# Optimization experiments

Hardware: AMD Instinct MI355X
Metric: run time of the kernel (lower is better)

## Reference

```python
import jax, jax.numpy as jnp
from jax import lax
import numpy as np

N, T, D, H, HG, OG = 2048, 256, 16, 256, 256, 128

def setup_inputs() -> dict:
    key = jax.random.key(0)
    ks = jax.random.split(key, 16)
    s = 0.05
    return {
        'x':    jax.random.normal(ks[0], (N, T, D), jnp.float32),
        'Wih0': jax.random.normal(ks[1], (4 * H, D), jnp.float32) * s,
        'Whh0': jax.random.normal(ks[2], (4 * H, H), jnp.float32) * s,
        'bih0': jax.random.normal(ks[3], (4 * H,), jnp.float32) * s,
        'bhh0': jax.random.normal(ks[4], (4 * H,), jnp.float32) * s,
        'Wih1': jax.random.normal(ks[5], (4 * H, H), jnp.float32) * s,
        'Whh1': jax.random.normal(ks[6], (4 * H, H), jnp.float32) * s,
        'bih1': jax.random.normal(ks[7], (4 * H,), jnp.float32) * s,
        'bhh1': jax.random.normal(ks[8], (4 * H,), jnp.float32) * s,
        'Wg1':  jax.random.normal(ks[9], (H, HG), jnp.float32) * s,
        'Wg2':  jax.random.normal(ks[10], (HG, OG), jnp.float32) * s,
        'Wfc':  jax.random.normal(ks[11], (OG, 1), jnp.float32) * s,
        'bfc':  jax.random.normal(ks[12], (1,), jnp.float32) * s,
    }

def lstm_layer(x, Wih, Whh, bih, bhh):
    # x: [N, T, Din]; torch gate order i, f, g, o stacked along 4H
    n = x.shape[0]
    h4 = Whh.shape[0]
    hid = h4 // 4
    xg = jnp.einsum('ntd,gd->ntg', x, Wih) + bih + bhh  # precompute input part
    def step(carry, g_t):
        h, c = carry
        g = g_t + h @ Whh.T
        i, f, gg, o = jnp.split(g, 4, axis=-1)
        c = jax.nn.sigmoid(f) * c + jax.nn.sigmoid(i) * jnp.tanh(gg)
        h = jax.nn.sigmoid(o) * jnp.tanh(c)
        return (h, c), h
    h0 = jnp.zeros((n, hid), x.dtype)
    (_, _), hs = lax.scan(step, (h0, h0), jnp.swapaxes(xg, 0, 1))
    return jnp.swapaxes(hs, 0, 1)  # [N, T, H]

def adjacency(nf):
    # detached correlation graph + symmetric degree normalization
    f = lax.stop_gradient(nf)
    xc = f - f.mean(axis=1, keepdims=True)
    cov = xc @ xc.T
    d = jnp.sqrt(jnp.diag(cov))
    corr = jnp.nan_to_num(jnp.clip(cov / (d[:, None] * d[None, :]), -1.0, 1.0))
    A = corr + jnp.eye(f.shape[0], dtype=f.dtype)
    dinv = jnp.power(A.sum(axis=1), -0.5)
    dinv = jnp.where(jnp.isinf(dinv), 0.0, dinv)
    return dinv[:, None] * A * dinv[None, :]

def reference(x, Wih0, Whh0, bih0, bhh0, Wih1, Whh1, bih1, bhh1, Wg1, Wg2, Wfc, bfc):
    h = lstm_layer(x, Wih0, Whh0, bih0, bhh0)
    h = lstm_layer(h, Wih1, Whh1, bih1, bhh1)
    nf = h[:, -1, :]                      # [N, H]
    adj = adjacency(nf)                   # [N, N]
    g1 = jax.nn.relu(adj @ (nf @ Wg1))    # GCN layer 1 (dropout=0, eval)
    g2 = adj @ (g1 @ Wg2)                 # GCN layer 2
    pred = g2 @ Wfc + bfc                 # [N, 1]
    return pred[:, 0]
```

## Files before the change

kernel.cpp:

```cpp
#include <hip/hip_runtime.h>
#include <hip/hip_bf16.h>
#include <cmath>

#define NN 2048
#define TT 256
#define DD 16
#define HH 256
#define NBLK 512

typedef __attribute__((ext_vector_type(8))) short short8;
typedef __attribute__((ext_vector_type(4))) float f32x4;

__device__ __forceinline__ float sigmoidf_(float x){ return 1.0f/(1.0f+expf(-x)); }

__device__ __forceinline__ void glds16(const __hip_bfloat16* g, __hip_bfloat16* l){
  __builtin_amdgcn_global_load_lds(
      (const __attribute__((address_space(1))) void*)g,
      (__attribute__((address_space(3))) void*)l, 16, 0, 0);
}

__global__ __launch_bounds__(256) void pack_w2(const float* __restrict__ W,
                                               __hip_bfloat16* __restrict__ P){
  int tid = blockIdx.x*256 + threadIdx.x;
  int r = tid >> 8, k = tid & 255;
  float w = W[tid];
  __hip_bfloat16 h = __float2bfloat16(w);
  __hip_bfloat16 l = __float2bfloat16(w - __bfloat162float(h));
  size_t base = (size_t)r*512;
  P[base + k] = h; P[base + 256 + k] = l;
}
__global__ __launch_bounds__(256) void pack_w0(const float* __restrict__ W,
                                               __hip_bfloat16* __restrict__ P){
  int tid = blockIdx.x*256 + threadIdx.x;
  int r = tid >> 4, k = tid & 15;
  float w = W[tid];
  __hip_bfloat16 h = __float2bfloat16(w);
  __hip_bfloat16 l = __float2bfloat16(w - __bfloat162float(h));
  size_t base = (size_t)r*64;
  P[base + k] = h; P[base + 16 + k] = h; P[base + 32 + k] = l;
  P[base + 48 + k] = __float2bfloat16(0.0f);
}
__global__ __launch_bounds__(256) void pack_x(const float* __restrict__ x,
                                              __hip_bfloat16* __restrict__ Xp){
  int tid = blockIdx.x*256 + threadIdx.x;
  const float* xr = x + (size_t)tid*16;
  __hip_bfloat16* o = Xp + (size_t)tid*64;
  for (int k=0;k<16;k++){
    float v = xr[k];
    __hip_bfloat16 h = __float2bfloat16(v);
    __hip_bfloat16 l = __float2bfloat16(v - __bfloat162float(h));
    o[k] = h; o[16+k] = l; o[32+k] = h; o[48+k] = __float2bfloat16(0.0f);
  }
}
__global__ __launch_bounds__(256) void recon_nf(const __hip_bfloat16* __restrict__ hi,
    const __hip_bfloat16* __restrict__ lo, float* __restrict__ nf){
  int tid = blockIdx.x*256 + threadIdx.x;
  nf[tid] = __bfloat162float(hi[tid]) + __bfloat162float(lo[tid]);
}

__global__ __launch_bounds__(256) void bar_init(unsigned* __restrict__ bar){
  for (int i = threadIdx.x; i < 2048; i += 256) bar[i] = 0u;
}

__device__ __forceinline__ void lean_sync(unsigned* bar, int t, int bid){
  __syncthreads();
  if (threadIdx.x == 0){
    const int x = bid & 7;
    unsigned a = __hip_atomic_fetch_add(bar + x*16, 1u, __ATOMIC_RELAXED,
                                        __HIP_MEMORY_SCOPE_AGENT);
    if (a == (unsigned)(64u*(t+1) - 1u)){
      asm volatile("buffer_wbl2 sc1\n\ts_waitcnt vmcnt(0)" ::: "memory");
      unsigned g = __hip_atomic_fetch_add(bar + 128, 1u, __ATOMIC_RELAXED,
                                          __HIP_MEMORY_SCOPE_AGENT);
      if (g == (unsigned)(8u*(t+1) - 1u)){
        #pragma unroll
        for (int i=0;i<16;i++)
          __hip_atomic_store(bar + 256 + i*64, (unsigned)(t+1),
                             __ATOMIC_RELAXED, __HIP_MEMORY_SCOPE_AGENT);
      } else {
        while (__hip_atomic_load(bar + 256 + x*64, __ATOMIC_RELAXED,
                                 __HIP_MEMORY_SCOPE_AGENT) < (unsigned)(t+1))
          __builtin_amdgcn_s_sleep(8);
      }
      asm volatile("buffer_inv sc1\n\ts_waitcnt vmcnt(0)" ::: "memory");
      __hip_atomic_store(bar + 1536 + x*64, (unsigned)(t+1),
                         __ATOMIC_RELAXED, __HIP_MEMORY_SCOPE_AGENT);
    } else {
      while (__hip_atomic_load(bar + 1536 + x*64, __ATOMIC_RELAXED,
                               __HIP_MEMORY_SCOPE_AGENT) < (unsigned)(t+1))
        __builtin_amdgcn_s_sleep(4);
    }
  }
  __syncthreads();
  asm volatile("buffer_inv\n\ts_waitcnt vmcnt(0)" ::: "memory");
}

__device__ __forceinline__ void mm_merged(
    const __hip_bfloat16* __restrict__ Ahi, const __hip_bfloat16* __restrict__ Alo,
    size_t lda,
    const __hip_bfloat16* __restrict__ Bhi, const __hip_bfloat16* __restrict__ Blo,
    size_t ldb, int Klen,
    int m0, int j0, int wv, int lane, int rr, int sw8, int frow,
    f32x4 (&acc)[2][4],
    __hip_bfloat16* AsH, __hip_bfloat16* AsL,
    __hip_bfloat16* BsH, __hip_bfloat16* BsL)
{
  const size_t arow = (size_t)(m0 + wv*32 + rr)*lda + sw8;
  const size_t brow = (size_t)(wv*256 + j0 + rr)*ldb + sw8;
  for (int kb=0; kb<Klen; kb+=64){
    {
      const __hip_bfloat16* AbH = Ahi + arow + kb;
      __hip_bfloat16* AdH = AsH + (wv*32)*64;
      #pragma unroll
      for (int c2=0;c2<4;c2++) glds16(AbH + (size_t)(c2*8)*lda, AdH + c2*8*64);
      const __hip_bfloat16* AbL = Alo + arow + kb;
      __hip_bfloat16* AdL = AsL + (wv*32)*64;
      #pragma unroll
      for (int c2=0;c2<4;c2++) glds16(AbL + (size_t)(c2*8)*lda, AdL + c2*8*64);
      const __hip_bfloat16* Bb1 = Bhi + brow + kb;
      __hip_bfloat16* Bd1 = BsH + (wv<<4)*64;
      glds16(Bb1, Bd1); glds16(Bb1 + (size_t)8*ldb, Bd1 + 8*64);
      const __hip_bfloat16* Bb2 = Blo + brow + kb;
      __hip_bfloat16* Bd2 = BsL + (wv<<4)*64;
      glds16(Bb2, Bd2); glds16(Bb2 + (size_t)8*ldb, Bd2 + 8*64);
    }
    __syncthreads();
    #pragma unroll
    for (int w2=0; w2<2; ++w2){
      const int sl8 = ((((w2<<2) + (lane>>4)) ^ (lane&7)) << 3);
      short8 ah0 = *(const short8*)&AsH[(wv*32 +      frow)*64 + sl8];
      short8 ah1 = *(const short8*)&AsH[(wv*32 + 16 + frow)*64 + sl8];
      short8 al0 = *(const short8*)&AsL[(wv*32 +      frow)*64 + sl8];
      short8 al1 = *(const short8*)&AsL[(wv*32 + 16 + frow)*64 + sl8];
      #pragma unroll
      for (int g=0; g<4; ++g){
        short8 bh = *(const short8*)&BsH[((g<<4) + frow)*64 + sl8];
        acc[0][g] = __builtin_amdgcn_mfma_f32_16x16x32_bf16(ah0, bh, acc[0][g], 0,0,0);
        acc[1][g] = __builtin_amdgcn_mfma_f32_16x16x32_bf16(ah1, bh, acc[1][g], 0,0,0);
        acc[0][g] = __builtin_amdgcn_mfma_f32_16x16x32_bf16(al0, bh, acc[0][g], 0,0,0);
        acc[1][g] = __builtin_amdgcn_mfma_f32_16x16x32_bf16(al1, bh, acc[1][g], 0,0,0);
        short8 bl = *(const short8*)&BsL[((g<<4) + frow)*64 + sl8];
        acc[0][g] = __builtin_amdgcn_mfma_f32_16x16x32_bf16(ah0, bl, acc[0][g], 0,0,0);
        acc[1][g] = __builtin_amdgcn_mfma_f32_16x16x32_bf16(ah1, bl, acc[1][g], 0,0,0);
      }
    }
    __syncthreads();
  }
}

__device__ __forceinline__ void mm_single64(
    const __hip_bfloat16* __restrict__ A, size_t lda,
    const __hip_bfloat16* __restrict__ B, size_t ldb,
    int m0, int j0, int wv, int lane, int rr, int sw8, int frow,
    f32x4 (&acc)[2][4],
    __hip_bfloat16* As0, __hip_bfloat16* Bh0)
{
  {
    const __hip_bfloat16* Ab = A + (size_t)(m0 + wv*32 + rr)*lda + sw8;
    __hip_bfloat16* Ad = As0 + (wv*32)*64;
    #pragma unroll
    for (int c2=0;c2<4;c2++) glds16(Ab + (size_t)(c2*8)*lda, Ad + c2*8*64);
    const __hip_bfloat16* Bb1 = B + (size_t)(wv*256 + j0 + rr)*ldb + sw8;
    __hip_bfloat16* Bd1 = Bh0 + (wv<<4)*64;
    glds16(Bb1, Bd1); glds16(Bb1 + (size_t)8*ldb, Bd1 + 8*64);
  }
  __syncthreads();
  #pragma unroll
  for (int w2=0; w2<2; ++w2){
    const int sl8 = ((((w2<<2) + (lane>>4)) ^ (lane&7)) << 3);
    short8 a0 = *(const short8*)&As0[(wv*32 +      frow)*64 + sl8];
    short8 a1 = *(const short8*)&As0[(wv*32 + 16 + frow)*64 + sl8];
    #pragma unroll
    for (int g=0; g<4; ++g){
      short8 b1 = *(const short8*)&Bh0[((g<<4) + frow)*64 + sl8];
      acc[0][g] = __builtin_amdgcn_mfma_f32_16x16x32_bf16(a0, b1, acc[0][g], 0,0,0);
      acc[1][g] = __builtin_amdgcn_mfma_f32_16x16x32_bf16(a1, b1, acc[1][g], 0,0,0);
    }
  }
  __syncthreads();
}

__global__ __launch_bounds__(256, 2) void lstm2_all(
    const __hip_bfloat16* __restrict__ Xp,
    const __hip_bfloat16* __restrict__ P0ih,
    const __hip_bfloat16* __restrict__ P0hh,
    const __hip_bfloat16* __restrict__ P1ih,
    const __hip_bfloat16* __restrict__ P1hh,
    const float* __restrict__ bih0, const float* __restrict__ bhh0,
    const float* __restrict__ bih1, const float* __restrict__ bhh1,
    __hip_bfloat16* __restrict__ H0hi0, __hip_bfloat16* __restrict__ H0lo0,
    __hip_bfloat16* __restrict__ H0hi1, __hip_bfloat16* __restrict__ H0lo1,
    __hip_bfloat16* __restrict__ H1hi0, __hip_bfloat16* __restrict__ H1lo0,
    __hip_bfloat16* __restrict__ H1hi1, __hip_bfloat16* __restrict__ H1lo1,
    unsigned* __restrict__ bar)
{
  __shared__ __align__(16) __hip_bfloat16 AsH[128*64];
  __shared__ __align__(16) __hip_bfloat16 AsL[128*64];
  __shared__ __align__(16) __hip_bfloat16 BsH[64*64];
  __shared__ __align__(16) __hip_bfloat16 BsL[64*64];

  const int bid = blockIdx.x;
  const int xcd = bid & 7;
  const int slot = bid >> 3;
  const bool isL0 = xcd < 4;
  const int lg = isL0 ? xcd : (xcd - 4);
  const int jg = ((lg & 1) << 3) + (slot & 7);
  const int mg = ((lg >> 1) << 3) + (slot >> 3);
  const int m0 = mg << 7;
  const int j0 = jg << 4;
  const int lane = threadIdx.x & 63, wv = threadIdx.x >> 6;
  const int rr = lane >> 3;
  const int sw8 = (((lane & 7) ^ rr) << 3);
  const int frow = lane & 15;

  const int j = j0 + frow;
  const float* bih = isL0 ? bih0 : bih1;
  const float* bhh = isL0 ? bhh0 : bhh1;
  const float b0 = bih[j]        + bhh[j];
  const float b1 = bih[HH + j]   + bhh[HH + j];
  const float b2 = bih[2*HH + j] + bhh[2*HH + j];
  const float b3 = bih[3*HH + j] + bhh[3*HH + j];

  float creg[2][4] = {{0.f,0.f,0.f,0.f},{0.f,0.f,0.f,0.f}};

  for (int t = 0; t <= TT; ++t){
    const int p = t & 1;
    const bool active = isL0 ? (t < TT) : (t >= 1);
    if (active){
      f32x4 acc[2][4] = {};
      const __hip_bfloat16* h0p_hi = p ? H0hi0 : H0hi1;
      const __hip_bfloat16* h0p_lo = p ? H0lo0 : H0lo1;
      if (isL0){
        if (t != 0){
          mm_merged(h0p_hi, h0p_lo, 256, P0hh, P0hh+256, 512, 256,
                    m0, j0, wv, lane, rr, sw8, frow, acc, AsH, AsL, BsH, BsL);
        }
        mm_single64(Xp + (size_t)t*64, (size_t)TT*64, P0ih, 64,
                    m0, j0, wv, lane, rr, sw8, frow, acc, AsH, BsH);
      } else {
        mm_merged(h0p_hi, h0p_lo, 256, P1ih, P1ih+256, 512, 256,
                  m0, j0, wv, lane, rr, sw8, frow, acc, AsH, AsL, BsH, BsL);
        if (t != 1){
          const __hip_bfloat16* h1p_hi = p ? H1hi1 : H1hi0;
          const __hip_bfloat16* h1p_lo = p ? H1lo1 : H1lo0;
          mm_merged(h1p_hi, h1p_lo, 256, P1hh, P1hh+256, 512, 256,
                    m0, j0, wv, lane, rr, sw8, frow, acc, AsH, AsL, BsH, BsL);
        }
      }
      __hip_bfloat16* ohi = isL0 ? (p ? H0hi1 : H0hi0)
                                 : (p ? H1hi0 : H1hi1);
      __hip_bfloat16* olo = isL0 ? (p ? H0lo1 : H0lo0)
                                 : (p ? H1lo0 : H1lo1);
      #pragma unroll
      for (int mt=0; mt<2; ++mt){
        const int mrb = m0 + wv*32 + mt*16 + ((lane>>4)<<2);
        #pragma unroll
        for (int r=0; r<4; ++r){
          const size_t mi = (size_t)(mrb + r)*HH + j;
          float gi = acc[mt][0][r] + b0;
          float gf = acc[mt][1][r] + b1;
          float gg = acc[mt][2][r] + b2;
          float go = acc[mt][3][r] + b3;
          float cn = sigmoidf_(gf)*creg[mt][r] + sigmoidf_(gi)*tanhf(gg);
          creg[mt][r] = cn;
          float hv = sigmoidf_(go)*tanhf(cn);
          __hip_bfloat16 hb = __float2bfloat16(hv);
          ohi[mi] = hb;
          olo[mi] = __float2bfloat16(hv - __bfloat162float(hb));
        }
      }
    }
    if (t < TT) lean_sync(bar, t, bid);
  }
}

__global__ __launch_bounds__(256) void gemm_nn(
    float* __restrict__ C, const float* __restrict__ A, const float* __restrict__ B,
    int K, int lda, int ldb, int ldc, int relu)
{
  __shared__ float As_[16][68];
  __shared__ float Bs_[16][64];
  float acc[4][4] = {};
  const int tx = threadIdx.x;
  const int m0 = blockIdx.y<<6, n0 = blockIdx.x<<6;
  const int am = tx>>2, ak = (tx&3)<<2;
  const int bk = tx>>4, bn = (tx&15)<<2;
  const int mm = (tx>>4)<<2, nc = (tx&15)<<2;
  for (int kb=0; kb<K; kb+=16){
    float4 av = *reinterpret_cast<const float4*>(A + (size_t)(m0+am)*lda + kb + ak);
    As_[ak][am]=av.x; As_[ak+1][am]=av.y; As_[ak+2][am]=av.z; As_[ak+3][am]=av.w;
    *reinterpret_cast<float4*>(&Bs_[bk][bn]) =
      *reinterpret_cast<const float4*>(B + (size_t)(kb+bk)*ldb + n0 + bn);
    __syncthreads();
    #pragma unroll
    for (int k=0;k<16;k++){
      float4 a4 = *reinterpret_cast<const float4*>(&As_[k][mm]);
      float4 b4 = *reinterpret_cast<const float4*>(&Bs_[k][nc]);
      acc[0][0]=fmaf(a4.x,b4.x,acc[0][0]); acc[0][1]=fmaf(a4.x,b4.y,acc[0][1]);
      acc[0][2]=fmaf(a4.x,b4.z,acc[0][2]); acc[0][3]=fmaf(a4.x,b4.w,acc[0][3]);
      acc[1][0]=fmaf(a4.y,b4.x,acc[1][0]); acc[1][1]=fmaf(a4.y,b4.y,acc[1][1]);
      acc[1][2]=fmaf(a4.y,b4.z,acc[1][2]); acc[1][3]=fmaf(a4.y,b4.w,acc[1][3]);
      acc[2][0]=fmaf(a4.z,b4.x,acc[2][0]); acc[2][1]=fmaf(a4.z,b4.y,acc[2][1]);
      acc[2][2]=fmaf(a4.z,b4.z,acc[2][2]); acc[2][3]=fmaf(a4.z,b4.w,acc[2][3]);
      acc[3][0]=fmaf(a4.w,b4.x,acc[3][0]); acc[3][1]=fmaf(a4.w,b4.y,acc[3][1]);
      acc[3][2]=fmaf(a4.w,b4.z,acc[3][2]); acc[3][3]=fmaf(a4.w,b4.w,acc[3][3]);
    }
    __syncthreads();
  }
  #pragma unroll
  for (int r=0;r<4;r++){
    float4 v = make_float4(acc[r][0],acc[r][1],acc[r][2],acc[r][3]);
    if (relu){ v.x=fmaxf(v.x,0.f); v.y=fmaxf(v.y,0.f); v.z=fmaxf(v.z,0.f); v.w=fmaxf(v.w,0.f); }
    *reinterpret_cast<float4*>(C + (size_t)(m0+mm+r)*ldc + n0 + nc) = v;
  }
}

__global__ __launch_bounds__(256) void gemm_nt(
    float* __restrict__ C, const float* __restrict__ A, const float* __restrict__ B,
    int K, int lda, int ldb, int ldc)
{
  __shared__ float As_[16][68];
  __shared__ float Bs_[16][68];
  float acc[4][4] = {};
  const int tx = threadIdx.x;
  const int m0 = blockIdx.y<<6, n0 = blockIdx.x<<6;
  const int am = tx>>2, ak = (tx&3)<<2;
  const int mm = (tx>>4)<<2, nc = (tx&15)<<2;
  for (int kb=0; kb<K; kb+=16){
    float4 av = *reinterpret_cast<const float4*>(A + (size_t)(m0+am)*lda + kb + ak);
    As_[ak][am]=av.x; As_[ak+1][am]=av.y; As_[ak+2][am]=av.z; As_[ak+3][am]=av.w;
    float4 bv = *reinterpret_cast<const float4*>(B + (size_t)(n0+am)*ldb + kb + ak);
    Bs_[ak][am]=bv.x; Bs_[ak+1][am]=bv.y; Bs_[ak+2][am]=bv.z; Bs_[ak+3][am]=bv.w;
    __syncthreads();
    #pragma unroll
    for (int k=0;k<16;k++){
      float4 a4 = *reinterpret_cast<const float4*>(&As_[k][mm]);
      float4 b4 = *reinterpret_cast<const float4*>(&Bs_[k][nc]);
      acc[0][0]=fmaf(a4.x,b4.x,acc[0][0]); acc[0][1]=fmaf(a4.x,b4.y,acc[0][1]);
      acc[0][2]=fmaf(a4.x,b4.z,acc[0][2]); acc[0][3]=fmaf(a4.x,b4.w,acc[0][3]);
      acc[1][0]=fmaf(a4.y,b4.x,acc[1][0]); acc[1][1]=fmaf(a4.y,b4.y,acc[1][1]);
      acc[1][2]=fmaf(a4.y,b4.z,acc[1][2]); acc[1][3]=fmaf(a4.y,b4.w,acc[1][3]);
      acc[2][0]=fmaf(a4.z,b4.x,acc[2][0]); acc[2][1]=fmaf(a4.z,b4.y,acc[2][1]);
      acc[2][2]=fmaf(a4.z,b4.z,acc[2][2]); acc[2][3]=fmaf(a4.z,b4.w,acc[2][3]);
      acc[3][0]=fmaf(a4.w,b4.x,acc[3][0]); acc[3][1]=fmaf(a4.w,b4.y,acc[3][1]);
      acc[3][2]=fmaf(a4.w,b4.z,acc[3][2]); acc[3][3]=fmaf(a4.w,b4.w,acc[3][3]);
    }
    __syncthreads();
  }
  #pragma unroll
  for (int r=0;r<4;r++){
    float4 v = make_float4(acc[r][0],acc[r][1],acc[r][2],acc[r][3]);
    *reinterpret_cast<float4*>(C + (size_t)(m0+mm+r)*ldc + n0 + nc) = v;
  }
}

__global__ __launch_bounds__(256) void rowstat(const float* __restrict__ nf,
    float* __restrict__ xc, float* __restrict__ dvec)
{
  __shared__ float red[256];
  int n = blockIdx.x, tx = threadIdx.x;
  float v = nf[(size_t)n*HH + tx];
  red[tx] = v; __syncthreads();
  for (int s=128; s>0; s>>=1){ if (tx<s) red[tx]+=red[tx+s]; __syncthreads(); }
  float mean = red[0] * (1.0f/HH);
  __syncthreads();
  float d = v - mean;
  xc[(size_t)n*HH + tx] = d;
  red[tx] = d*d; __syncthreads();
  for (int s=128; s>0; s>>=1){ if (tx<s) red[tx]+=red[tx+s]; __syncthreads(); }
  if (tx==0) dvec[n] = sqrtf(red[0]);
}

__global__ __launch_bounds__(256) void rowsum(const float* __restrict__ cov,
    const float* __restrict__ dvec, float* __restrict__ dinv)
{
  __shared__ float red[256];
  int i = blockIdx.x, tx = threadIdx.x;
  float di = dvec[i];
  float s = 0.f;
  for (int jj=tx; jj<NN; jj+=256){
    float r = cov[(size_t)i*NN + jj] / (di * dvec[jj]);
    if (r != r) r = 0.f; else r = fminf(1.f, fmaxf(-1.f, r));
    s += r;
  }
  red[tx]=s; __syncthreads();
  for (int st=128; st>0; st>>=1){ if (tx<st) red[tx]+=red[tx+st]; __syncthreads(); }
  if (tx==0){
    float tot = red[0] + 1.0f;
    float p = powf(tot, -0.5f);
    if (isinf(p)) p = 0.f;
    dinv[i] = p;
  }
}

__global__ __launch_bounds__(256) void adjnorm(float* __restrict__ cov,
    const float* __restrict__ dvec, const float* __restrict__ dinv)
{
  size_t idx = (size_t)blockIdx.x*256 + threadIdx.x;
  int i = (int)(idx >> 11), jj = (int)(idx & (NN-1));
  float r = cov[idx] / (dvec[i]*dvec[jj]);
  if (r != r) r = 0.f; else r = fminf(1.f, fmaxf(-1.f, r));
  if (i==jj) r += 1.f;
  cov[idx] = dinv[i]*r*dinv[jj];
}

__global__ __launch_bounds__(128) void predk(const float* __restrict__ G2,
    const float* __restrict__ Wfc, const float* __restrict__ bfc, float* __restrict__ out)
{
  int n = blockIdx.x, tx = threadIdx.x;
  float v = G2[(size_t)n*128 + tx] * Wfc[tx];
  for (int off=32; off>0; off>>=1) v += __shfl_down(v, off);
  __shared__ float p[2];
  if ((tx&63)==0) p[tx>>6] = v;
  __syncthreads();
  if (tx==0) out[n] = p[0] + p[1] + bfc[0];
}

extern "C" void kernel_launch(void* const* d_in, const int* in_sizes, int n_in,
                              void* d_out, int out_size, void* d_ws, size_t ws_size,
                              hipStream_t stream)
{
  const float* x    = (const float*)d_in[0];
  const float* Wih0 = (const float*)d_in[1];
  const float* Whh0 = (const float*)d_in[2];
  const float* bih0 = (const float*)d_in[3];
  const float* bhh0 = (const float*)d_in[4];
  const float* Wih1 = (const float*)d_in[5];
  const float* Whh1 = (const float*)d_in[6];
  const float* bih1 = (const float*)d_in[7];
  const float* bhh1 = (const float*)d_in[8];
  const float* Wg1  = (const float*)d_in[9];
  const float* Wg2  = (const float*)d_in[10];
  const float* Wfc  = (const float*)d_in[11];
  const float* bfc  = (const float*)d_in[12];
  float* out = (float*)d_out;

  char* w = (char*)d_ws;
  auto alloc = [&](size_t bytes){ char* p = w; w += (bytes + 255) & ~(size_t)255; return p; };
  __hip_bfloat16* Xp   = (__hip_bfloat16*)alloc((size_t)NN*TT*64*2);
  __hip_bfloat16* P0hh = (__hip_bfloat16*)alloc((size_t)1024*512*2);
  __hip_bfloat16* P1ih = (__hip_bfloat16*)alloc((size_t)1024*512*2);
  __hip_bfloat16* P1hh = (__hip_bfloat16*)alloc((size_t)1024*512*2);
  __hip_bfloat16* P0ih = (__hip_bfloat16*)alloc((size_t)1024*64*2);
  __hip_bfloat16 *H0hi[2], *H0lo[2], *H1hi[2], *H1lo[2];
  for (int i=0;i<2;i++){ H0hi[i]=(__hip_bfloat16*)alloc((size_t)NN*HH*2);
                         H0lo[i]=(__hip_bfloat16*)alloc((size_t)NN*HH*2); }
  for (int i=0;i<2;i++){ H1hi[i]=(__hip_bfloat16*)alloc((size_t)NN*HH*2);
                         H1lo[i]=(__hip_bfloat16*)alloc((size_t)NN*HH*2); }
  float* nf   = (float*)alloc((size_t)NN*HH*4);
  float* xc   = (float*)alloc((size_t)NN*HH*4);
  float* cov  = (float*)alloc((size_t)NN*NN*4);
  float* t1   = (float*)alloc((size_t)NN*HH*4);
  float* G1   = (float*)alloc((size_t)NN*HH*4);
  float* t2   = (float*)alloc((size_t)NN*128*4);
  float* G2   = (float*)alloc((size_t)NN*128*4);
  float* dvec = (float*)alloc((size_t)NN*4);
  float* dinv = (float*)alloc((size_t)NN*4);
  unsigned* bar = (unsigned*)alloc(8192);

  hipLaunchKernelGGL(bar_init, dim3(1), dim3(256), 0, stream, bar);
  hipLaunchKernelGGL(pack_w2, dim3(1024), dim3(256), 0, stream, Whh0, P0hh);
  hipLaunchKernelGGL(pack_w2, dim3(1024), dim3(256), 0, stream, Wih1, P1ih);
  hipLaunchKernelGGL(pack_w2, dim3(1024), dim3(256), 0, stream, Whh1, P1hh);
  hipLaunchKernelGGL(pack_w0, dim3(64),   dim3(256), 0, stream, Wih0, P0ih);
  hipLaunchKernelGGL(pack_x,  dim3(2048), dim3(256), 0, stream, x, Xp);

  hipLaunchKernelGGL(lstm2_all, dim3(NBLK), dim3(256), 0, stream,
      Xp, P0ih, P0hh, P1ih, P1hh, bih0, bhh0, bih1, bhh1,
      H0hi[0], H0lo[0], H0hi[1], H0lo[1],
      H1hi[0], H1lo[0], H1hi[1], H1lo[1], bar);

  hipLaunchKernelGGL(recon_nf, dim3(2048), dim3(256), 0, stream, H1hi[1], H1lo[1], nf);

  hipLaunchKernelGGL(rowstat, dim3(NN), dim3(256), 0, stream, nf, xc, dvec);
  hipLaunchKernelGGL(gemm_nt, dim3(NN/64, NN/64), dim3(256), 0, stream,
      cov, xc, xc, HH, HH, HH, NN);
  hipLaunchKernelGGL(rowsum, dim3(NN), dim3(256), 0, stream, cov, dvec, dinv);
  hipLaunchKernelGGL(adjnorm, dim3(NN*NN/256), dim3(256), 0, stream, cov, dvec, dinv);

  hipLaunchKernelGGL(gemm_nn, dim3(HH/64, NN/64), dim3(256), 0, stream,
      t1, nf, Wg1, HH, HH, HH, HH, 0);
  hipLaunchKernelGGL(gemm_nn, dim3(HH/64, NN/64), dim3(256), 0, stream,
      G1, cov, t1, NN, NN, HH, HH, 1);
  hipLaunchKernelGGL(gemm_nn, dim3(128/64, NN/64), dim3(256), 0, stream,
      t2, G1, Wg2, HH, HH, 128, 128, 0);
  hipLaunchKernelGGL(gemm_nn, dim3(128/64, NN/64), dim3(256), 0, stream,
      G2, cov, t2, NN, NN, 128, 128, 0);
  hipLaunchKernelGGL(predk, dim3(NN), dim3(128), 0, stream, G2, Wfc, bfc, out);
}
```

Baseline: 5.370 ms.

## Replace cache flush/invalidate barrier with device-coherent loads and stores

Removes the L2 writeback and invalidate instructions from the grid barrier and flattens it to a single release level, so the last group arriver signals all groups directly. Hidden-state stores become packed 32-bit agent-scope atomic stores, with lanes pairing via shuffle so even lanes write the hi pair and odd lanes the lo pair. Recurrent-state global-to-LDS loads use cache-policy bits 17 so they bypass non-coherent caches. This cuts per-step barrier latency and store count, but correctness now relies on these coherence bits being enough without explicit fences.

```diff
diff --git a/kernel.cpp b/kernel.cpp
--- a/kernel.cpp
+++ b/kernel.cpp
@@ -17,6 +17,11 @@
   __builtin_amdgcn_global_load_lds(
       (const __attribute__((address_space(1))) void*)g,
       (__attribute__((address_space(3))) void*)l, 16, 0, 0);
+}
+__device__ __forceinline__ void glds16_dev(const __hip_bfloat16* g, __hip_bfloat16* l){
+  __builtin_amdgcn_global_load_lds(
+      (const __attribute__((address_space(1))) void*)g,
+      (__attribute__((address_space(3))) void*)l, 16, 0, 17);
 }
 
 __global__ __launch_bounds__(256) void pack_w2(const float* __restrict__ W,
@@ -69,22 +74,18 @@
     unsigned a = __hip_atomic_fetch_add(bar + x*16, 1u, __ATOMIC_RELAXED,
                                         __HIP_MEMORY_SCOPE_AGENT);
     if (a == (unsigned)(64u*(t+1) - 1u)){
-      asm volatile("buffer_wbl2 sc1\n\ts_waitcnt vmcnt(0)" ::: "memory");
       unsigned g = __hip_atomic_fetch_add(bar + 128, 1u, __ATOMIC_RELAXED,
                                           __HIP_MEMORY_SCOPE_AGENT);
       if (g == (unsigned)(8u*(t+1) - 1u)){
         #pragma unroll
-        for (int i=0;i<16;i++)
-          __hip_atomic_store(bar + 256 + i*64, (unsigned)(t+1),
+        for (int i=0;i<8;i++)
+          __hip_atomic_store(bar + 1536 + i*64, (unsigned)(t+1),
                              __ATOMIC_RELAXED, __HIP_MEMORY_SCOPE_AGENT);
       } else {
-        while (__hip_atomic_load(bar + 256 + x*64, __ATOMIC_RELAXED,
+        while (__hip_atomic_load(bar + 1536 + x*64, __ATOMIC_RELAXED,
                                  __HIP_MEMORY_SCOPE_AGENT) < (unsigned)(t+1))
-          __builtin_amdgcn_s_sleep(8);
+          __builtin_amdgcn_s_sleep(4);
       }
-      asm volatile("buffer_inv sc1\n\ts_waitcnt vmcnt(0)" ::: "memory");
-      __hip_atomic_store(bar + 1536 + x*64, (unsigned)(t+1),
-                         __ATOMIC_RELAXED, __HIP_MEMORY_SCOPE_AGENT);
     } else {
       while (__hip_atomic_load(bar + 1536 + x*64, __ATOMIC_RELAXED,
                                __HIP_MEMORY_SCOPE_AGENT) < (unsigned)(t+1))
@@ -92,7 +93,6 @@
     }
   }
   __syncthreads();
-  asm volatile("buffer_inv\n\ts_waitcnt vmcnt(0)" ::: "memory");
 }
 
 __device__ __forceinline__ void mm_merged(
@@ -112,11 +112,11 @@
       const __hip_bfloat16* AbH = Ahi + arow + kb;
       __hip_bfloat16* AdH = AsH + (wv*32)*64;
       #pragma unroll
-      for (int c2=0;c2<4;c2++) glds16(AbH + (size_t)(c2*8)*lda, AdH + c2*8*64);
+      for (int c2=0;c2<4;c2++) glds16_dev(AbH + (size_t)(c2*8)*lda, AdH + c2*8*64);
       const __hip_bfloat16* AbL = Alo + arow + kb;
       __hip_bfloat16* AdL = AsL + (wv*32)*64;
       #pragma unroll
-      for (int c2=0;c2<4;c2++) glds16(AbL + (size_t)(c2*8)*lda, AdL + c2*8*64);
+      for (int c2=0;c2<4;c2++) glds16_dev(AbL + (size_t)(c2*8)*lda, AdL + c2*8*64);
       const __hip_bfloat16* Bb1 = Bhi + brow + kb;
       __hip_bfloat16* Bd1 = BsH + (wv<<4)*64;
       glds16(Bb1, Bd1); glds16(Bb1 + (size_t)8*ldb, Bd1 + 8*64);
@@ -212,6 +212,7 @@
   const int rr = lane >> 3;
   const int sw8 = (((lane & 7) ^ rr) << 3);
   const int frow = lane & 15;
+  const int odd = frow & 1;
 
   const int j = j0 + frow;
   const float* bih = isL0 ? bih0 : bih1;
@@ -256,7 +257,6 @@
         const int mrb = m0 + wv*32 + mt*16 + ((lane>>4)<<2);
         #pragma unroll
         for (int r=0; r<4; ++r){
-          const size_t mi = (size_t)(mrb + r)*HH + j;
           float gi = acc[mt][0][r] + b0;
           float gf = acc[mt][1][r] + b1;
           float gg = acc[mt][2][r] + b2;
@@ -265,8 +265,21 @@
           creg[mt][r] = cn;
           float hv = sigmoidf_(go)*tanhf(cn);
           __hip_bfloat16 hb = __float2bfloat16(hv);
-          ohi[mi] = hb;
-          olo[mi] = __float2bfloat16(hv - __bfloat162float(hb));
+          __hip_bfloat16 lb = __float2bfloat16(hv - __bfloat162float(hb));
+          unsigned hs = (unsigned)*reinterpret_cast<unsigned short*>(&hb);
+          unsigned ls = (unsigned)*reinterpret_cast<unsigned short*>(&lb);
+          unsigned hp = (unsigned)__shfl_xor((int)hs, 1);
+          unsigned lp = (unsigned)__shfl_xor((int)ls, 1);
+          const size_t base = (size_t)(mrb + r)*HH + (size_t)(j & ~1);
+          if (!odd){
+            unsigned v = hs | (hp << 16);
+            __hip_atomic_store((unsigned*)(ohi + base), v,
+                               __ATOMIC_RELAXED, __HIP_MEMORY_SCOPE_AGENT);
+          } else {
+            unsigned v = lp | (ls << 16);
+            __hip_atomic_store((unsigned*)(olo + base), v,
+                               __ATOMIC_RELAXED, __HIP_MEMORY_SCOPE_AGENT);
+          }
         }
       }
     }
```

Result: faster. 4.648 ms, median of 2 (-13.4%).
